# Kernel optimization log

Measured on AMD Instinct MI355X. Metric: run time of the kernel, lower is better.

## Reference

```python
import math
import jax, jax.numpy as jnp
import numpy as np

NUM_HEADS = 16
BASE = 10000.0


def _rope_sin_cos(seq_len, head_dim):
    # theta_j = pos / base^(2j/dim), j in [0, dim//2)
    j = jnp.arange(head_dim // 2, dtype=jnp.float32)
    inv_freq = jnp.power(jnp.float32(BASE), -2.0 * j / head_dim)  # [d/2]
    pos = jnp.arange(seq_len, dtype=jnp.float32)
    ang = pos[:, None] * inv_freq[None, :]          # [S, d/2]
    sin, cos = jnp.sin(ang), jnp.cos(ang)
    # interleave-repeat each entry twice: [S, d]
    sin2 = jnp.stack([sin, sin], axis=-1).reshape(seq_len, head_dim)
    cos2 = jnp.stack([cos, cos], axis=-1).reshape(seq_len, head_dim)
    return sin2, cos2


def _apply_rope(x, sin2, cos2):
    # x: [B, H, S, d]; rotate-half interleaved: (-x1, x0, -x3, x2, ...)
    x_even, x_odd = x[..., 0::2], x[..., 1::2]
    rot = jnp.stack([-x_odd, x_even], axis=-1).reshape(x.shape)
    return x * cos2 + rot * sin2


def setup_inputs() -> dict:
    key = jax.random.key(0)
    ks = jax.random.split(key, 9)
    B, S, H = 2, 2048, 2048
    sc = 1.0 / math.sqrt(H)
    return {
        "hidden_state": jax.random.normal(ks[0], (B, S, H), jnp.float32),
        "Wq": jax.random.normal(ks[1], (H, H), jnp.float32) * sc,
        "bq": jax.random.normal(ks[2], (H,), jnp.float32) * 0.01,
        "Wk": jax.random.normal(ks[3], (H, H), jnp.float32) * sc,
        "bk": jax.random.normal(ks[4], (H,), jnp.float32) * 0.01,
        "Wv": jax.random.normal(ks[5], (H, H), jnp.float32) * sc,
        "bv": jax.random.normal(ks[6], (H,), jnp.float32) * 0.01,
        "Wo": jax.random.normal(ks[7], (H, H), jnp.float32) * sc,
        "bo": jax.random.normal(ks[8], (H,), jnp.float32) * 0.01,
    }


def reference(hidden_state, Wq, bq, Wk, bk, Wv, bv, Wo, bo):
    B, S, H = hidden_state.shape
    nh = NUM_HEADS
    hd = H // nh

    def proj(W, b):
        y = jnp.einsum('bsh,hd->bsd', hidden_state, W) + b
        return y.reshape(B, S, nh, hd).transpose(0, 2, 1, 3)  # [B,nh,S,hd]

    q = proj(Wq, bq)
    k = proj(Wk, bk)
    v = proj(Wv, bv)

    sin2, cos2 = _rope_sin_cos(S, hd)  # [S, hd]
    q = _apply_rope(q, sin2, cos2)
    k = _apply_rope(k, sin2, cos2)

    scale = 1.0 / math.sqrt(hd)
    attn = jnp.einsum('bhqd,bhkd->bhqk', q, k) * scale  # [B,nh,S,S]
    attn = jax.nn.softmax(attn, axis=-1)
    out = jnp.einsum('bhqk,bhkd->bhqd', attn, v)
    out = out.transpose(0, 2, 1, 3).reshape(B, S, H)
    return jnp.einsum('bsh,hd->bsd', out, Wo) + bo
```

## Files before the change

kernel.cpp:

```cpp
#include <hip/hip_runtime.h>
#include <math.h>


typedef __bf16 bf16;
typedef __attribute__((ext_vector_type(8))) __bf16 bf16x8;
typedef __attribute__((ext_vector_type(4))) __bf16 bf16x4;
typedef __attribute__((ext_vector_type(4))) float f32x4;

#define S_LEN 2048
#define NHEAD 16
#define HD 128

__device__ __forceinline__ f32x4 mfma16(bf16x8 a, bf16x8 b, f32x4 c) {
    return __builtin_amdgcn_mfma_f32_16x16x32_bf16(a, b, c, 0, 0, 0);
}

__device__ __forceinline__ void gload16(const bf16* g, bf16* s) {
    __builtin_amdgcn_global_load_lds(
        (const __attribute__((address_space(1))) void*)g,
        (__attribute__((address_space(3))) void*)s, 16, 0, 0);
}

#define BAR()                                  \
    do {                                       \
        asm volatile("" ::: "memory");         \
        __builtin_amdgcn_s_barrier();          \
        asm volatile("" ::: "memory");         \
    } while (0)
#define WAITV(n) asm volatile("s_waitcnt vmcnt(" #n ")" ::: "memory")
#define SCHED0() __builtin_amdgcn_sched_barrier(0)

__global__ __launch_bounds__(256) void cvt_f32_bf16(const float* __restrict__ x,
                                                    bf16* __restrict__ y, int n) {
    int i = (blockIdx.x * 256 + threadIdx.x) * 4;
    if (i + 3 < n) {
        const float4 v = *(const float4*)(x + i);
        bf16x4 o;
        o[0] = (bf16)v.x; o[1] = (bf16)v.y; o[2] = (bf16)v.z; o[3] = (bf16)v.w;
        *(bf16x4*)(y + i) = o;
    }
}

__global__ __launch_bounds__(128) void rope_tables(float* __restrict__ st,
                                                   float* __restrict__ ct) {
    const int s = blockIdx.x, d = threadIdx.x;
    const float invf = exp2f(-0.20762050593046013f * (float)(d >> 1));
    float sn, cs;
    sincosf((float)s * invf, &sn, &cs);
    st[(s << 7) | d] = sn;
    ct[(s << 7) | d] = cs;
}

__global__ __launch_bounds__(256) void transpose_cvt(const float* __restrict__ W,
                                                     bf16* __restrict__ Wt,
                                                     int Kd, int Nd) {
    __shared__ float tile[32][33];
    const int tx = threadIdx.x & 31, ty = threadIdx.x >> 5;
    const int bn = blockIdx.x * 32, bk = blockIdx.y * 32;
#pragma unroll
    for (int r = 0; r < 32; r += 8)
        tile[ty + r][tx] = W[(size_t)(bk + ty + r) * Nd + bn + tx];
    __syncthreads();
#pragma unroll
    for (int r = 0; r < 32; r += 8)
        Wt[(size_t)(bn + ty + r) * Kd + bk + tx] = (bf16)tile[tx][ty + r];
}

#define STG_A(kt, reg)                                                        \
    do {                                                                      \
        bf16* d_ = smem + (((((kt) & 1) << 1) + (reg)) << 13);                \
        const size_t ko_ = (size_t)((kt) << 6) + ((size_t)(reg) << 17);       \
        gload16(A + aoff0 + ko_, d_ + loff0);                                 \
        gload16(A + aoff1 + ko_, d_ + loff1);                                 \
    } while (0)
#define STG_B(kt, reg)                                                        \
    do {                                                                      \
        bf16* d_ = smem + 32768 + (((((kt) & 1) << 1) + (reg)) << 13);        \
        const size_t ko_ = (size_t)((kt) << 6) + ((size_t)(reg) << 16);       \
        gload16(Bt + boff0 + ko_, d_ + loff0);                                \
        gload16(Bt + boff1 + ko_, d_ + loff1);                                \
    } while (0)

__global__ __launch_bounds__(512, 2)
void gemm_qkv(const bf16* __restrict__ A, const bf16* __restrict__ Bt,
              const float* __restrict__ bq, const float* __restrict__ bk,
              const float* __restrict__ bv, bf16* __restrict__ Qo,
              bf16* __restrict__ Ko, bf16* __restrict__ Vo,
              const float* __restrict__ stab, const float* __restrict__ ctab) {
    __shared__ __align__(16) bf16 smem[65536];
    const int tid = threadIdx.x;
    const int w = tid >> 6, l = tid & 63;
    const int lr = l & 15, lq = l >> 4;
    const int wr = w >> 2, wc = w & 3;
    const int m0 = blockIdx.y * 256, n0 = blockIdx.x * 256;

    size_t aoff0, aoff1, boff0, boff1;
    {
        const int ch0 = tid, ch1 = 512 + tid;
        const int rl0 = ch0 >> 3, rl1 = ch1 >> 3;
        const int cc0 = (ch0 & 7) ^ (rl0 & 7), cc1 = (ch1 & 7) ^ (rl1 & 7);
        aoff0 = (size_t)(m0 + (rl0 & 63) + ((rl0 >> 6) << 7)) * 2048 + (cc0 << 3);
        aoff1 = (size_t)(m0 + (rl1 & 63) + ((rl1 >> 6) << 7)) * 2048 + (cc1 << 3);
        boff0 = (size_t)(n0 + (rl0 & 31) + ((rl0 >> 5) << 6)) * 2048 + (cc0 << 3);
        boff1 = (size_t)(n0 + (rl1 & 31) + ((rl1 >> 5) << 6)) * 2048 + (cc1 << 3);
    }
    const int loff0 = tid << 3, loff1 = 4096 + (tid << 3);

    f32x4 acc[8][4];
    const f32x4 fz = {0.f, 0.f, 0.f, 0.f};
#pragma unroll
    for (int i = 0; i < 8; ++i)
#pragma unroll
        for (int j = 0; j < 4; ++j) acc[i][j] = fz;

    STG_A(0, 0); STG_B(0, 0); STG_B(0, 1); STG_A(0, 1);
    STG_A(1, 0); STG_B(1, 0); STG_A(1, 1);
    WAITV(6);
    BAR();

    const int csel0 = ((0 * 4 + lq) ^ (lr & 7)) << 3;
    const int csel1 = ((1 * 4 + lq) ^ (lr & 7)) << 3;
    const int arow = (wr * 64 + lr) << 6;
    const int brow = (wc * 32 + lr) << 6;

#pragma unroll 2
    for (int t = 0; t < 32; ++t) {
        const int buf = t & 1;
        const int abase = (buf << 1) << 13;
        const int bbase = 32768 + ((buf << 1) << 13);
        bf16x8 a[4][2], b0[2][2], b1[2][2];

#pragma unroll
        for (int i = 0; i < 4; ++i) {
            a[i][0] = *(const bf16x8*)&smem[abase + arow + (i << 10) + csel0];
            a[i][1] = *(const bf16x8*)&smem[abase + arow + (i << 10) + csel1];
        }
#pragma unroll
        for (int j = 0; j < 2; ++j) {
            b0[j][0] = *(const bf16x8*)&smem[bbase + brow + (j << 10) + csel0];
            b0[j][1] = *(const bf16x8*)&smem[bbase + brow + (j << 10) + csel1];
        }
        if (t + 1 < 32) STG_B(t + 1, 1);
        BAR();
        SCHED0();
        __builtin_amdgcn_s_setprio(1);
#pragma unroll
        for (int i = 0; i < 4; ++i)
#pragma unroll
            for (int j = 0; j < 2; ++j) {
                acc[i][j] = mfma16(a[i][0], b0[j][0], acc[i][j]);
                acc[i][j] = mfma16(a[i][1], b0[j][1], acc[i][j]);
            }
        __builtin_amdgcn_s_setprio(0);
        SCHED0();
        BAR();

#pragma unroll
        for (int j = 0; j < 2; ++j) {
            b1[j][0] = *(const bf16x8*)&smem[bbase + 8192 + brow + (j << 10) + csel0];
            b1[j][1] = *(const bf16x8*)&smem[bbase + 8192 + brow + (j << 10) + csel1];
        }
        if (t + 2 < 32) STG_A(t + 2, 0);
        BAR();
        SCHED0();
        __builtin_amdgcn_s_setprio(1);
#pragma unroll
        for (int i = 0; i < 4; ++i)
#pragma unroll
            for (int j = 0; j < 2; ++j) {
                acc[i][2 + j] = mfma16(a[i][0], b1[j][0], acc[i][2 + j]);
                acc[i][2 + j] = mfma16(a[i][1], b1[j][1], acc[i][2 + j]);
            }
        __builtin_amdgcn_s_setprio(0);
        SCHED0();
        BAR();

#pragma unroll
        for (int i = 0; i < 4; ++i) {
            a[i][0] = *(const bf16x8*)&smem[abase + 8192 + arow + (i << 10) + csel0];
            a[i][1] = *(const bf16x8*)&smem[abase + 8192 + arow + (i << 10) + csel1];
        }
        if (t + 2 < 32) STG_B(t + 2, 0);
        BAR();
        SCHED0();
        __builtin_amdgcn_s_setprio(1);
#pragma unroll
        for (int i = 0; i < 4; ++i)
#pragma unroll
            for (int j = 0; j < 2; ++j) {
                acc[4 + i][2 + j] = mfma16(a[i][0], b1[j][0], acc[4 + i][2 + j]);
                acc[4 + i][2 + j] = mfma16(a[i][1], b1[j][1], acc[4 + i][2 + j]);
            }
        __builtin_amdgcn_s_setprio(0);
        SCHED0();
        BAR();

        if (t + 2 < 32) STG_A(t + 2, 1);
        BAR();
        SCHED0();
        __builtin_amdgcn_s_setprio(1);
#pragma unroll
        for (int i = 0; i < 4; ++i)
#pragma unroll
            for (int j = 0; j < 2; ++j) {
                acc[4 + i][j] = mfma16(a[i][0], b0[j][0], acc[4 + i][j]);
                acc[4 + i][j] = mfma16(a[i][1], b0[j][1], acc[4 + i][j]);
            }
        __builtin_amdgcn_s_setprio(0);
        SCHED0();
        if (t + 2 < 32) {
            WAITV(6);
        } else if (t + 1 < 32) {
            WAITV(0);
        }
        BAR();
    }

    const int seg = n0 >> 11;
    const float* bias = (seg == 0) ? bq : (seg == 1) ? bk : bv;
    if (seg == 2) {
        bf16* lt = smem + w * 4608;
        const int cgb = (n0 & 2047) + wc * 64;
        const int h = cgb >> 7, d0 = cgb & 127;
        const int b = m0 >> 11;
        const int sb = (m0 & 2047) + wr * 128;
#pragma unroll
        for (int mh = 0; mh < 2; ++mh) {
#pragma unroll
            for (int mi = 0; mi < 4; ++mi)
#pragma unroll
                for (int nj = 0; nj < 4; ++nj) {
                    const int cl = ((nj >> 1) << 5) + ((nj & 1) << 4) + lr;
                    const float bv_ = bias[cgb + cl];
#pragma unroll
                    for (int r = 0; r < 4; ++r)
                        lt[cl * 72 + mi * 16 + lq * 4 + r] =
                            (bf16)(acc[mh * 4 + mi][nj][r] + bv_);
                }
#pragma unroll
            for (int p = 0; p < 8; ++p) {
                const int dl = p * 8 + (l >> 3);
                const int sc = l & 7;
                const bf16x8 v = *(const bf16x8*)&lt[dl * 72 + sc * 8];
                *(bf16x8*)&Vo[((size_t)((b << 4) | h) * HD + d0 + dl) * S_LEN +
                              sb + mh * 64 + sc * 8] = v;
            }
        }
    } else {
        bf16* outB = (seg == 0) ? Qo : Ko;
#pragma unroll
        for (int mi = 0; mi < 8; ++mi) {
            const int rg0 = m0 + wr * 128 + ((mi >> 2) << 6) + ((mi & 3) << 4) + (lq << 2);
#pragma unroll
            for (int nj = 0; nj < 4; ++nj) {
                const int cg2 = (n0 & 2047) + wc * 64 + ((nj >> 1) << 5) +
                                ((nj & 1) << 4) + lr;
                const float bv_ = bias[cg2];
                const int h = cg2 >> 7, d = cg2 & 127;
#pragma unroll
                for (int r = 0; r < 4; ++r) {
                    const int rg = rg0 + r;
                    const int b = rg >> 11, s = rg & 2047;
                    float v = acc[mi][nj][r] + bv_;
                    float p = __shfl_xor(v, 1);
                    const float sn = stab[(s << 7) | d];
                    const float cs = ctab[(s << 7) | d];
                    float o = (d & 1) ? (v * cs + p * sn) : (v * cs - p * sn);
                    if (seg == 0) o *= 0.08838834764831843f;
                    outB[((size_t)((b << 4) + h) * S_LEN + s) * HD + d] = (bf16)o;
                }
            }
        }
    }
}

__global__ __launch_bounds__(256, 3)
void gemm_out(const bf16* __restrict__ A, const bf16* __restrict__ Bt,
              const float* __restrict__ bias, float* __restrict__ outF,
              int M, int N, int K) {
    __shared__ __align__(16) bf16 As[128 * 64];
    __shared__ __align__(16) bf16 Bs[128 * 64];
    const int t = threadIdx.x;
    const int w = t >> 6, l = t & 63;
    const int lr = l & 15, lq = l >> 4;
    const int m0 = blockIdx.y * 128, n0 = blockIdx.x * 128;
    const int wm = (w >> 1) * 64, wn = (w & 1) * 64;

    f32x4 acc[4][4];
    const f32x4 fz = {0.f, 0.f, 0.f, 0.f};
#pragma unroll
    for (int i = 0; i < 4; ++i)
#pragma unroll
        for (int j = 0; j < 4; ++j) acc[i][j] = fz;

    bf16x8 rA[4], rB[4];
#pragma unroll
    for (int c = 0; c < 4; ++c) {
        const int chunk = c * 256 + t;
        const int row = chunk >> 3, cc = chunk & 7;
        rA[c] = *(const bf16x8*)&A[(size_t)(m0 + row) * K + cc * 8];
        rB[c] = *(const bf16x8*)&Bt[(size_t)(n0 + row) * K + cc * 8];
    }

    for (int k0 = 0; k0 < K; k0 += 64) {
#pragma unroll
        for (int c = 0; c < 4; ++c) {
            const int chunk = c * 256 + t;
            const int row = chunk >> 3, cc = chunk & 7;
            const int d = (row * 8 + (cc ^ (row & 7))) * 8;
            *(bf16x8*)&As[d] = rA[c];
            *(bf16x8*)&Bs[d] = rB[c];
        }
        __syncthreads();
        if (k0 + 64 < K) {
#pragma unroll
            for (int c = 0; c < 4; ++c) {
                const int chunk = c * 256 + t;
                const int row = chunk >> 3, cc = chunk & 7;
                rA[c] = *(const bf16x8*)&A[(size_t)(m0 + row) * K + k0 + 64 + cc * 8];
                rB[c] = *(const bf16x8*)&Bt[(size_t)(n0 + row) * K + k0 + 64 + cc * 8];
            }
        }
#pragma unroll
        for (int s = 0; s < 2; ++s) {
            bf16x8 af[4], bfr[4];
#pragma unroll
            for (int i = 0; i < 4; ++i) {
                const int row = wm + i * 16 + lr;
                af[i] = *(const bf16x8*)&As[(row * 8 + ((s * 4 + lq) ^ (row & 7))) * 8];
            }
#pragma unroll
            for (int j = 0; j < 4; ++j) {
                const int row = wn + j * 16 + lr;
                bfr[j] = *(const bf16x8*)&Bs[(row * 8 + ((s * 4 + lq) ^ (row & 7))) * 8];
            }
#pragma unroll
            for (int i = 0; i < 4; ++i)
#pragma unroll
                for (int j = 0; j < 4; ++j)
                    acc[i][j] = mfma16(af[i], bfr[j], acc[i][j]);
        }
        __syncthreads();
    }
#pragma unroll
    for (int i = 0; i < 4; ++i) {
        const int rg0 = m0 + wm + i * 16 + lq * 4;
#pragma unroll
        for (int j = 0; j < 4; ++j) {
            const int cg = n0 + wn + j * 16 + lr;
            const float bv = bias[cg];
#pragma unroll
            for (int r = 0; r < 4; ++r)
                outF[(size_t)(rg0 + r) * N + cg] = acc[i][j][r] + bv;
        }
    }
}

__global__ __launch_bounds__(256, 2)
void attn_fwd(const bf16* __restrict__ Q, const bf16* __restrict__ K,
              const bf16* __restrict__ Vt, bf16* __restrict__ AO) {
    __shared__ __align__(16) bf16 Ks[64 * 128];
    __shared__ __align__(16) bf16 Vs[128 * 64];
    const int t = threadIdx.x;
    const int w = t >> 6, l = t & 63;
    const int lr = l & 15, lq = l >> 4;
    const int blk = blockIdx.x;
    const int qt = (blk >> 3) & 15;
    const int bh = ((blk & 7) << 2) | (blk >> 7);
    const int b = bh >> 4, h = bh & 15;

    const bf16* Qp = Q + (size_t)bh * S_LEN * HD;
    const bf16* Kp = K + (size_t)bh * S_LEN * HD;
    const bf16* Vp = Vt + (size_t)bh * HD * S_LEN;

    bf16x8 qf[2][4];
#pragma unroll
    for (int i = 0; i < 2; ++i)
#pragma unroll
        for (int s = 0; s < 4; ++s)
            qf[i][s] = *(const bf16x8*)&Qp[(size_t)(qt * 128 + w * 32 + i * 16 + lr) * HD +
                                           s * 32 + lq * 8];

    f32x4 O[2][8];
    const f32x4 fz = {0.f, 0.f, 0.f, 0.f};
#pragma unroll
    for (int i = 0; i < 2; ++i)
#pragma unroll
        for (int jd = 0; jd < 8; ++jd) O[i][jd] = fz;
    float lst[2][4] = {{0.f, 0.f, 0.f, 0.f}, {0.f, 0.f, 0.f, 0.f}};

    bf16x8 rK[4], rV[4];
#pragma unroll
    for (int c = 0; c < 4; ++c) {
        const int chunk = c * 256 + t;
        const int kr = chunk >> 4, kc = chunk & 15;
        const int vr = chunk >> 3, vc = chunk & 7;
        rK[c] = *(const bf16x8*)&Kp[(size_t)kr * HD + kc * 8];
        rV[c] = *(const bf16x8*)&Vp[(size_t)vr * S_LEN + vc * 8];
    }

    for (int kt = 0; kt < 32; ++kt) {
#pragma unroll
        for (int c = 0; c < 4; ++c) {
            const int chunk = c * 256 + t;
            const int kr = chunk >> 4, kc = chunk & 15;
            const int vr = chunk >> 3, vc = chunk & 7;
            *(bf16x8*)&Ks[(kr * 16 + (kc ^ (kr & 15))) * 8] = rK[c];
            *(bf16x8*)&Vs[(vr * 8 + (vc ^ (vr & 7))) * 8] = rV[c];
        }
        __syncthreads();

        if (kt < 31) {
#pragma unroll
            for (int c = 0; c < 4; ++c) {
                const int chunk = c * 256 + t;
                const int kr = chunk >> 4, kc = chunk & 15;
                const int vr = chunk >> 3, vc = chunk & 7;
                rK[c] = *(const bf16x8*)&Kp[(size_t)((kt + 1) * 64 + kr) * HD + kc * 8];
                rV[c] = *(const bf16x8*)&Vp[(size_t)vr * S_LEN + (kt + 1) * 64 + vc * 8];
            }
        }

        f32x4 Sc[2][4];
#pragma unroll
        for (int i = 0; i < 2; ++i)
#pragma unroll
            for (int j = 0; j < 4; ++j) Sc[i][j] = fz;
#pragma unroll
        for (int s = 0; s < 4; ++s) {
            bf16x8 kf[4];
#pragma unroll
            for (int j = 0; j < 4; ++j) {
                const int krow = j * 16 + lr;
                kf[j] = *(const bf16x8*)&Ks[(krow * 16 + ((s * 4 + lq) ^ (krow & 15))) * 8];
            }
#pragma unroll
            for (int i = 0; i < 2; ++i)
#pragma unroll
                for (int j = 0; j < 4; ++j)
                    Sc[i][j] = mfma16(qf[i][s], kf[j], Sc[i][j]);
        }
        __syncthreads();

        bf16* Ps = Ks;
#pragma unroll
        for (int i = 0; i < 2; ++i)
#pragma unroll
            for (int j = 0; j < 4; ++j)
#pragma unroll
                for (int r = 0; r < 4; ++r) {
                    const float p = __expf(Sc[i][j][r]);
                    lst[i][r] += p;
                    const int prow = w * 32 + i * 16 + lq * 4 + r;
                    const int pch = (j * 2 + (lr >> 3)) ^ (prow & 7);
                    Ps[(prow * 8 + pch) * 8 + (lr & 7)] = (bf16)p;
                }

#pragma unroll
        for (int s = 0; s < 2; ++s) {
            bf16x8 pf[2], vf[8];
#pragma unroll
            for (int i = 0; i < 2; ++i) {
                const int prow = w * 32 + i * 16 + lr;
                pf[i] = *(const bf16x8*)&Ps[(prow * 8 + ((s * 4 + lq) ^ (prow & 7))) * 8];
            }
#pragma unroll
            for (int jd = 0; jd < 8; ++jd) {
                const int vrow = jd * 16 + lr;
                vf[jd] = *(const bf16x8*)&Vs[(vrow * 8 + ((s * 4 + lq) ^ (vrow & 7))) * 8];
            }
#pragma unroll
            for (int i = 0; i < 2; ++i)
#pragma unroll
                for (int jd = 0; jd < 8; ++jd)
                    O[i][jd] = mfma16(pf[i], vf[jd], O[i][jd]);
        }
        __syncthreads();
    }

#pragma unroll
    for (int mask = 1; mask < 16; mask <<= 1)
#pragma unroll
        for (int i = 0; i < 2; ++i)
#pragma unroll
            for (int r = 0; r < 4; ++r) lst[i][r] += __shfl_xor(lst[i][r], mask);

#pragma unroll
    for (int i = 0; i < 2; ++i)
#pragma unroll
        for (int jd = 0; jd < 8; ++jd)
#pragma unroll
            for (int r = 0; r < 4; ++r) {
                const int srow = qt * 128 + w * 32 + i * 16 + lq * 4 + r;
                const float v = O[i][jd][r] / lst[i][r];
                AO[(size_t)(b * S_LEN + srow) * 2048 + h * HD + jd * 16 + lr] = (bf16)v;
            }
}

extern "C" void kernel_launch(void* const* d_in, const int* in_sizes, int n_in,
                              void* d_out, int out_size, void* d_ws, size_t ws_size,
                              hipStream_t stream) {
    const float* hs = (const float*)d_in[0];
    const float* Wq = (const float*)d_in[1];
    const float* bq = (const float*)d_in[2];
    const float* Wk = (const float*)d_in[3];
    const float* bk = (const float*)d_in[4];
    const float* Wv = (const float*)d_in[5];
    const float* bv = (const float*)d_in[6];
    const float* Wo = (const float*)d_in[7];
    const float* bo = (const float*)d_in[8];
    float* out = (float*)d_out;

    char* ws = (char*)d_ws;
    bf16* Xb = (bf16*)ws;
    bf16* Wt3 = (bf16*)(ws + (size_t)16777216);
    bf16* Qb = (bf16*)(ws + (size_t)41943040);
    bf16* Kb = (bf16*)(ws + (size_t)58720256);
    bf16* Vb = (bf16*)(ws + (size_t)75497472);
    float* stab = (float*)(ws + (size_t)92274688);
    float* ctab = (float*)(ws + (size_t)93323264);
    bf16* AO = Xb;

    const dim3 tg(64, 64);

    rope_tables<<<2048, 128, 0, stream>>>(stab, ctab);
    cvt_f32_bf16<<<8192, 256, 0, stream>>>(hs, Xb, 8388608);
    transpose_cvt<<<tg, 256, 0, stream>>>(Wq, Wt3, 2048, 2048);
    transpose_cvt<<<tg, 256, 0, stream>>>(Wk, Wt3 + (size_t)2048 * 2048, 2048, 2048);
    transpose_cvt<<<tg, 256, 0, stream>>>(Wv, Wt3 + (size_t)2 * 2048 * 2048, 2048, 2048);
    gemm_qkv<<<dim3(24, 16), 512, 0, stream>>>(Xb, Wt3, bq, bk, bv, Qb, Kb, Vb,
                                               stab, ctab);
    attn_fwd<<<512, 256, 0, stream>>>(Qb, Kb, Vb, AO);
    transpose_cvt<<<tg, 256, 0, stream>>>(Wo, Wt3, 2048, 2048);
    gemm_out<<<dim3(16, 32), 256, 0, stream>>>(AO, Wt3, bo, out, 4096, 2048, 2048);
}
```

Baseline: 403.0 us.

## Shrink QKV GEMM tile to 256x128 and simplify pipeline stages

After: 402.3 us. Within noise of the previous version (-0.2%).

```diff
diff --git a/kernel.cpp b/kernel.cpp
--- a/kernel.cpp
+++ b/kernel.cpp
@@ -28,7 +28,6 @@
         asm volatile("" ::: "memory");         \
     } while (0)
 #define WAITV(n) asm volatile("s_waitcnt vmcnt(" #n ")" ::: "memory")
-#define SCHED0() __builtin_amdgcn_sched_barrier(0)
 
 __global__ __launch_bounds__(256) void cvt_f32_bf16(const float* __restrict__ x,
                                                     bf16* __restrict__ y, int n) {
@@ -69,14 +68,14 @@
 #define STG_A(kt, reg)                                                        \
     do {                                                                      \
         bf16* d_ = smem + (((((kt) & 1) << 1) + (reg)) << 13);                \
-        const size_t ko_ = (size_t)((kt) << 6) + ((size_t)(reg) << 17);       \
+        const size_t ko_ = (size_t)((kt) << 6) + ((size_t)(reg) << 16);       \
         gload16(A + aoff0 + ko_, d_ + loff0);                                 \
         gload16(A + aoff1 + ko_, d_ + loff1);                                 \
     } while (0)
-#define STG_B(kt, reg)                                                        \
+#define STG_B(kt)                                                             \
     do {                                                                      \
-        bf16* d_ = smem + 32768 + (((((kt) & 1) << 1) + (reg)) << 13);        \
-        const size_t ko_ = (size_t)((kt) << 6) + ((size_t)(reg) << 16);       \
+        bf16* d_ = smem + 32768 + (((kt) & 1) << 13);                         \
+        const size_t ko_ = (size_t)((kt) << 6);                               \
         gload16(Bt + boff0 + ko_, d_ + loff0);                                \
         gload16(Bt + boff1 + ko_, d_ + loff1);                                \
     } while (0)
@@ -87,131 +86,96 @@
               const float* __restrict__ bv, bf16* __restrict__ Qo,
               bf16* __restrict__ Ko, bf16* __restrict__ Vo,
               const float* __restrict__ stab, const float* __restrict__ ctab) {
-    __shared__ __align__(16) bf16 smem[65536];
+    __shared__ __align__(16) bf16 smem[49152];
     const int tid = threadIdx.x;
     const int w = tid >> 6, l = tid & 63;
     const int lr = l & 15, lq = l >> 4;
-    const int wr = w >> 2, wc = w & 3;
-    const int m0 = blockIdx.y * 256, n0 = blockIdx.x * 256;
+    const int wr = w >> 1, wc = w & 1;
+    const int m0 = blockIdx.y * 256, n0 = blockIdx.x * 128;
 
     size_t aoff0, aoff1, boff0, boff1;
     {
         const int ch0 = tid, ch1 = 512 + tid;
         const int rl0 = ch0 >> 3, rl1 = ch1 >> 3;
         const int cc0 = (ch0 & 7) ^ (rl0 & 7), cc1 = (ch1 & 7) ^ (rl1 & 7);
-        aoff0 = (size_t)(m0 + (rl0 & 63) + ((rl0 >> 6) << 7)) * 2048 + (cc0 << 3);
-        aoff1 = (size_t)(m0 + (rl1 & 63) + ((rl1 >> 6) << 7)) * 2048 + (cc1 << 3);
-        boff0 = (size_t)(n0 + (rl0 & 31) + ((rl0 >> 5) << 6)) * 2048 + (cc0 << 3);
-        boff1 = (size_t)(n0 + (rl1 & 31) + ((rl1 >> 5) << 6)) * 2048 + (cc1 << 3);
+        aoff0 = (size_t)(m0 + ((rl0 >> 5) << 6) + (rl0 & 31)) * 2048 + (cc0 << 3);
+        aoff1 = (size_t)(m0 + ((rl1 >> 5) << 6) + (rl1 & 31)) * 2048 + (cc1 << 3);
+        boff0 = (size_t)(n0 + rl0) * 2048 + (cc0 << 3);
+        boff1 = (size_t)(n0 + rl1) * 2048 + (cc1 << 3);
     }
     const int loff0 = tid << 3, loff1 = 4096 + (tid << 3);
 
-    f32x4 acc[8][4];
+    f32x4 acc[4][4];
     const f32x4 fz = {0.f, 0.f, 0.f, 0.f};
 #pragma unroll
-    for (int i = 0; i < 8; ++i)
+    for (int i = 0; i < 4; ++i)
 #pragma unroll
         for (int j = 0; j < 4; ++j) acc[i][j] = fz;
 
-    STG_A(0, 0); STG_B(0, 0); STG_B(0, 1); STG_A(0, 1);
-    STG_A(1, 0); STG_B(1, 0); STG_A(1, 1);
+    STG_A(0, 0); STG_B(0); STG_A(0, 1); STG_A(1, 0); STG_B(1);
     WAITV(6);
     BAR();
 
     const int csel0 = ((0 * 4 + lq) ^ (lr & 7)) << 3;
     const int csel1 = ((1 * 4 + lq) ^ (lr & 7)) << 3;
-    const int arow = (wr * 64 + lr) << 6;
-    const int brow = (wc * 32 + lr) << 6;
+    const int aoffL = (wr * 32 + lr) << 6;
+    const int boffL = (wc * 64 + lr) << 6;
 
 #pragma unroll 2
     for (int t = 0; t < 32; ++t) {
         const int buf = t & 1;
         const int abase = (buf << 1) << 13;
-        const int bbase = 32768 + ((buf << 1) << 13);
-        bf16x8 a[4][2], b0[2][2], b1[2][2];
-
-#pragma unroll
-        for (int i = 0; i < 4; ++i) {
-            a[i][0] = *(const bf16x8*)&smem[abase + arow + (i << 10) + csel0];
-            a[i][1] = *(const bf16x8*)&smem[abase + arow + (i << 10) + csel1];
-        }
-#pragma unroll
-        for (int j = 0; j < 2; ++j) {
-            b0[j][0] = *(const bf16x8*)&smem[bbase + brow + (j << 10) + csel0];
-            b0[j][1] = *(const bf16x8*)&smem[bbase + brow + (j << 10) + csel1];
-        }
-        if (t + 1 < 32) STG_B(t + 1, 1);
+        const int bbase = 32768 + (buf << 13);
+        bf16x8 a[2][2], b[4][2];
+
+#pragma unroll
+        for (int i = 0; i < 2; ++i) {
+            a[i][0] = *(const bf16x8*)&smem[abase + aoffL + (i << 10) + csel0];
+            a[i][1] = *(const bf16x8*)&smem[abase + aoffL + (i << 10) + csel1];
+        }
+#pragma unroll
+        for (int j = 0; j < 4; ++j) {
+            b[j][0] = *(const bf16x8*)&smem[bbase + boffL + (j << 10) + csel0];
+            b[j][1] = *(const bf16x8*)&smem[bbase + boffL + (j << 10) + csel1];
+        }
+        if (t < 31) STG_A(t + 1, 1);
         BAR();
-        SCHED0();
         __builtin_amdgcn_s_setprio(1);
 #pragma unroll
-        for (int i = 0; i < 4; ++i)
-#pragma unroll
-            for (int j = 0; j < 2; ++j) {
-                acc[i][j] = mfma16(a[i][0], b0[j][0], acc[i][j]);
-                acc[i][j] = mfma16(a[i][1], b0[j][1], acc[i][j]);
+        for (int i = 0; i < 2; ++i)
+#pragma unroll
+            for (int j = 0; j < 4; ++j) {
+                acc[i][j] = mfma16(a[i][0], b[j][0], acc[i][j]);
+                acc[i][j] = mfma16(a[i][1], b[j][1], acc[i][j]);
             }
         __builtin_amdgcn_s_setprio(0);
-        SCHED0();
+        if (t < 31) {
+            WAITV(6);
+        } else {
+            WAITV(0);
+        }
         BAR();
 
 #pragma unroll
-        for (int j = 0; j < 2; ++j) {
-            b1[j][0] = *(const bf16x8*)&smem[bbase + 8192 + brow + (j << 10) + csel0];
-            b1[j][1] = *(const bf16x8*)&smem[bbase + 8192 + brow + (j << 10) + csel1];
-        }
-        if (t + 2 < 32) STG_A(t + 2, 0);
+        for (int i = 0; i < 2; ++i) {
+            a[i][0] = *(const bf16x8*)&smem[abase + 8192 + aoffL + (i << 10) + csel0];
+            a[i][1] = *(const bf16x8*)&smem[abase + 8192 + aoffL + (i << 10) + csel1];
+        }
+        if (t < 30) { STG_A(t + 2, 0); STG_B(t + 2); }
         BAR();
-        SCHED0();
         __builtin_amdgcn_s_setprio(1);
 #pragma unroll
-        for (int i = 0; i < 4; ++i)
-#pragma unroll
-            for (int j = 0; j < 2; ++j) {
-                acc[i][2 + j] = mfma16(a[i][0], b1[j][0], acc[i][2 + j]);
-                acc[i][2 + j] = mfma16(a[i][1], b1[j][1], acc[i][2 + j]);
+        for (int i = 0; i < 2; ++i)
+#pragma unroll
+            for (int j = 0; j < 4; ++j) {
+                acc[2 + i][j] = mfma16(a[i][0], b[j][0], acc[2 + i][j]);
+                acc[2 + i][j] = mfma16(a[i][1], b[j][1], acc[2 + i][j]);
             }
         __builtin_amdgcn_s_setprio(0);
-        SCHED0();
-        BAR();
-
-#pragma unroll
-        for (int i = 0; i < 4; ++i) {
-            a[i][0] = *(const bf16x8*)&smem[abase + 8192 + arow + (i << 10) + csel0];
-            a[i][1] = *(const bf16x8*)&smem[abase + 8192 + arow + (i << 10) + csel1];
-        }
-        if (t + 2 < 32) STG_B(t + 2, 0);
-        BAR();
-        SCHED0();
-        __builtin_amdgcn_s_setprio(1);
-#pragma unroll
-        for (int i = 0; i < 4; ++i)
-#pragma unroll
-            for (int j = 0; j < 2; ++j) {
-                acc[4 + i][2 + j] = mfma16(a[i][0], b1[j][0], acc[4 + i][2 + j]);
-                acc[4 + i][2 + j] = mfma16(a[i][1], b1[j][1], acc[4 + i][2 + j]);
-            }
-        __builtin_amdgcn_s_setprio(0);
-        SCHED0();
-        BAR();
-
-        if (t + 2 < 32) STG_A(t + 2, 1);
-        BAR();
-        SCHED0();
-        __builtin_amdgcn_s_setprio(1);
-#pragma unroll
-        for (int i = 0; i < 4; ++i)
-#pragma unroll
-            for (int j = 0; j < 2; ++j) {
-                acc[4 + i][j] = mfma16(a[i][0], b0[j][0], acc[4 + i][j]);
-                acc[4 + i][j] = mfma16(a[i][1], b0[j][1], acc[4 + i][j]);
-            }
-        __builtin_amdgcn_s_setprio(0);
-        SCHED0();
-        if (t + 2 < 32) {
+        if (t < 30) {
             WAITV(6);
-        } else if (t + 1 < 32) {
-            WAITV(0);
+        } else if (t == 30) {
+            WAITV(2);
         }
         BAR();
     }
@@ -223,45 +187,40 @@
         const int cgb = (n0 & 2047) + wc * 64;
         const int h = cgb >> 7, d0 = cgb & 127;
         const int b = m0 >> 11;
-        const int sb = (m0 & 2047) + wr * 128;
-#pragma unroll
-        for (int mh = 0; mh < 2; ++mh) {
-#pragma unroll
-            for (int mi = 0; mi < 4; ++mi)
-#pragma unroll
-                for (int nj = 0; nj < 4; ++nj) {
-                    const int cl = ((nj >> 1) << 5) + ((nj & 1) << 4) + lr;
-                    const float bv_ = bias[cgb + cl];
-#pragma unroll
-                    for (int r = 0; r < 4; ++r)
-                        lt[cl * 72 + mi * 16 + lq * 4 + r] =
-                            (bf16)(acc[mh * 4 + mi][nj][r] + bv_);
-                }
-#pragma unroll
-            for (int p = 0; p < 8; ++p) {
-                const int dl = p * 8 + (l >> 3);
-                const int sc = l & 7;
-                const bf16x8 v = *(const bf16x8*)&lt[dl * 72 + sc * 8];
-                *(bf16x8*)&Vo[((size_t)((b << 4) | h) * HD + d0 + dl) * S_LEN +
-                              sb + mh * 64 + sc * 8] = v;
-            }
+        const int sb = (m0 & 2047) + wr * 64;
+#pragma unroll
+        for (int i = 0; i < 4; ++i)
+#pragma unroll
+            for (int j = 0; j < 4; ++j) {
+                const int cl = j * 16 + lr;
+                const float bv_ = bias[cgb + cl];
+#pragma unroll
+                for (int r = 0; r < 4; ++r)
+                    lt[cl * 72 + i * 16 + lq * 4 + r] = (bf16)(acc[i][j][r] + bv_);
+            }
+#pragma unroll
+        for (int p = 0; p < 8; ++p) {
+            const int dl = p * 8 + (l >> 3);
+            const int sc = l & 7;
+            const bf16x8 v = *(const bf16x8*)&lt[dl * 72 + sc * 8];
+            *(bf16x8*)&Vo[((size_t)((b << 4) | h) * HD + d0 + dl) * S_LEN +
+                          sb + sc * 8] = v;
         }
     } else {
         bf16* outB = (seg == 0) ? Qo : Ko;
 #pragma unroll
-        for (int mi = 0; mi < 8; ++mi) {
-            const int rg0 = m0 + wr * 128 + ((mi >> 2) << 6) + ((mi & 3) << 4) + (lq << 2);
-#pragma unroll
-            for (int nj = 0; nj < 4; ++nj) {
-                const int cg2 = (n0 & 2047) + wc * 64 + ((nj >> 1) << 5) +
-                                ((nj & 1) << 4) + lr;
+        for (int i = 0; i < 4; ++i) {
+            const int rg0 = m0 + wr * 64 + i * 16 + lq * 4;
+#pragma unroll
+            for (int j = 0; j < 4; ++j) {
+                const int cg2 = (n0 & 2047) + wc * 64 + j * 16 + lr;
                 const float bv_ = bias[cg2];
                 const int h = cg2 >> 7, d = cg2 & 127;
 #pragma unroll
                 for (int r = 0; r < 4; ++r) {
                     const int rg = rg0 + r;
                     const int b = rg >> 11, s = rg & 2047;
-                    float v = acc[mi][nj][r] + bv_;
+                    float v = acc[i][j][r] + bv_;
                     float p = __shfl_xor(v, 1);
                     const float sn = stab[(s << 7) | d];
                     const float cs = ctab[(s << 7) | d];
@@ -528,7 +487,7 @@
     transpose_cvt<<<tg, 256, 0, stream>>>(Wq, Wt3, 2048, 2048);
     transpose_cvt<<<tg, 256, 0, stream>>>(Wk, Wt3 + (size_t)2048 * 2048, 2048, 2048);
     transpose_cvt<<<tg, 256, 0, stream>>>(Wv, Wt3 + (size_t)2 * 2048 * 2048, 2048, 2048);
-    gemm_qkv<<<dim3(24, 16), 512, 0, stream>>>(Xb, Wt3, bq, bk, bv, Qb, Kb, Vb,
+    gemm_qkv<<<dim3(48, 16), 512, 0, stream>>>(Xb, Wt3, bq, bk, bv, Qb, Kb, Vb,
                                                stab, ctab);
     attn_fwd<<<512, 256, 0, stream>>>(Qb, Kb, Vb, AO);
     transpose_cvt<<<tg, 256, 0, stream>>>(Wo, Wt3, 2048, 2048);
```
